# Kernel optimization log

Hardware: AMD Instinct MI355X
Metric: run time of the kernel (lower is better)

## Reference

```python
import jax, jax.numpy as jnp
import numpy as np

B, T, E, NH = 2, 2048, 512, 8
HD = E // NH
SCALE = float(HD) ** -0.5


def setup_inputs() -> dict:
    key = jax.random.key(0)
    ks = jax.random.split(key, 7)
    s = 0.02
    return {
        "x": jax.random.normal(ks[0], (B, T, E), dtype=jnp.float32),
        "w_qkv": jax.random.normal(ks[1], (E, 3 * E), dtype=jnp.float32) * s,
        "b_qkv": jax.random.normal(ks[2], (3 * E,), dtype=jnp.float32) * s,
        "w_od": jax.random.normal(ks[3], (E, 2 * NH), dtype=jnp.float32) * s,
        "b_od": jax.random.normal(ks[4], (2 * NH,), dtype=jnp.float32) * s,
        "w_out": jax.random.normal(ks[5], (E, E), dtype=jnp.float32) * s,
        "b_out": jax.random.normal(ks[6], (E,), dtype=jnp.float32) * s,
    }


def _heads(t):  # (B,T,E) -> (B*NH, T, HD)
    return t.reshape(B, T, NH, HD).transpose(0, 2, 1, 3).reshape(B * NH, T, HD)


def _point_mask(idx, j):  # idx: (B*NH,T) float indices -> one-hot (B*NH,T,T)
    return (j[None, None, :] == idx[:, :, None]).astype(jnp.float32)


def reference(x, w_qkv, b_qkv, w_od, b_od, w_out, b_out):
    qkv = x @ w_qkv + b_qkv
    Q, K, V = jnp.split(qkv, 3, axis=-1)  # each (B,T,E)

    od = Q @ w_od + b_od  # (B,T,2*NH)
    offset, duration = jnp.split(od, 2, axis=-1)
    offset = jnp.tanh(offset) * T
    duration = jax.nn.sigmoid(duration) * T

    query_index = jnp.arange(T, dtype=x.dtype)[None, :, None]  # (1,T,1)
    anchor = query_index + offset  # (B,T,NH)
    # 'b t nh -> (b nh) t'
    anchor = anchor.transpose(0, 2, 1).reshape(B * NH, T)
    duration = duration.transpose(0, 2, 1).reshape(B * NH, T)

    start = anchor - duration
    end = anchor + duration
    bound_l = jnp.floor(start)
    bound_r = jnp.ceil(end)
    anchor_l = jnp.floor(anchor)
    anchor_r = anchor_l + 1.0

    j = jnp.arange(T, dtype=x.dtype)
    neg_bound_weight = (bound_l - start)[:, :, None] * _point_mask(bound_l, j) \
                     + (end - bound_r)[:, :, None] * _point_mask(bound_r, j)
    anchor_dist_l = anchor - anchor_l
    anchor_weight = anchor_dist_l[:, :, None] * _point_mask(anchor_r, j) \
                  + (1.0 - anchor_dist_l)[:, :, None] * _point_mask(anchor_l, j)
    point_weight = 1.0 + neg_bound_weight + anchor_weight  # (B*NH,T,T)

    # segment mask: True OUTSIDE [bound_l, bound_r]
    attn_mask = (j[None, None, :] < bound_l[:, :, None]) | (j[None, None, :] > bound_r[:, :, None])

    Qh, Kh, Vh = _heads(Q), _heads(K), _heads(V)  # (B*NH, T, HD)
    scores = jnp.einsum('bic,brc->bir', Qh, Kh) * SCALE * point_weight
    scores = jnp.where(attn_mask, jnp.asarray(-1e8, scores.dtype), scores)
    attn = jax.nn.softmax(scores, axis=-1)
    out = jnp.einsum('bir,brc->bic', attn, Vh)  # (B*NH,T,HD)
    out = out.reshape(B, NH, T, HD).transpose(0, 2, 1, 3).reshape(B, T, E)
    return out @ w_out + b_out
```

## Files before the change

### kernel.cpp

```cpp
#include <hip/hip_runtime.h>
#include <math.h>

typedef float vf4 __attribute__((ext_vector_type(4)));
typedef float f32x4 __attribute__((ext_vector_type(4)));
typedef short bf16x8 __attribute__((ext_vector_type(8)));
typedef short short4v __attribute__((ext_vector_type(4)));
typedef int int2v __attribute__((ext_vector_type(2)));
typedef int int4v __attribute__((ext_vector_type(4)));

constexpr int B = 2, T = 2048, E = 512, NH = 8, HD = 64;
constexpr int BH = B * NH;
constexpr int NT = BH * T;
constexpr float SCALE = 0.125f;
constexpr float LOG2E = 1.44269504088896f;
constexpr float QSC = SCALE * LOG2E;

static __device__ __forceinline__ short f2bf(float f) {
  unsigned u = __float_as_uint(f);
  unsigned r = (u + 0x7fffu + ((u >> 16) & 1u)) >> 16;
  return (short)r;
}
static __device__ __forceinline__ unsigned pk2bf(float a, float b) {
  unsigned lo = (unsigned)(unsigned short)f2bf(a);
  unsigned hi = (unsigned)(unsigned short)f2bf(b);
  return lo | (hi << 16);
}
static __device__ __forceinline__ unsigned pkhu(float a, float b) {
  unsigned ua = __float_as_uint(a) + 0x8000u;
  unsigned ub = __float_as_uint(b) + 0x8000u;
  return __builtin_amdgcn_perm(ub, ua, 0x07060302u);
}
#if __has_builtin(__builtin_amdgcn_exp2f)
#define EXP2F(x) __builtin_amdgcn_exp2f(x)
#else
#define EXP2F(x) exp2f(x)
#endif
static __device__ __forceinline__ float bf2f(short s) {
  return __uint_as_float(((unsigned)(unsigned short)s) << 16);
}

__global__ __launch_bounds__(256) void prep_all(
    const float* __restrict__ x, const float* __restrict__ w_qkv,
    const float* __restrict__ b_qkv, const float* __restrict__ w_od,
    const float* __restrict__ b_od,
    short* __restrict__ xb, short* __restrict__ wTq, short* __restrict__ wTo,
    const float* __restrict__ w_out, float* __restrict__ Wc,
    float* __restrict__ bc)
{
  __shared__ float sh[8464];
  const int bid = blockIdx.x;
  const int tid = threadIdx.x;

  if (bid < 2048) {
    int idx = (bid * 256 + tid) * 4;
    vf4 v = *(const vf4*)&x[idx];
    short4v o;
    o[0] = f2bf(v[0]); o[1] = f2bf(v[1]); o[2] = f2bf(v[2]); o[3] = f2bf(v[3]);
    *(short4v*)&xb[idx] = o;
  } else if (bid < 3072) {
    const float* w; short* wT; int N, t;
    if (bid < 2816) { t = bid - 2048; w = w_qkv; wT = wTq; N = 1536; }
    else            { t = bid - 2816; w = w_out; wT = wTo; N = 512; }
    float (*tt)[33] = (float(*)[33])sh;
    const int k0 = (t & 15) * 32;
    const int n0 = (t >> 4) * 32;
    const int c = tid & 31, r = tid >> 5;
#pragma unroll
    for (int p = 0; p < 4; ++p)
      tt[r + p * 8][c] = w[(size_t)(k0 + r + p * 8) * N + n0 + c];
    __syncthreads();
#pragma unroll
    for (int p = 0; p < 4; ++p)
      wT[(size_t)(n0 + r + p * 8) * 512 + k0 + c] = f2bf(tt[c][r + p * 8]);
  } else {
    float* Lod = sh;
    float (*pb)[17] = (float(*)[17])(sh + 8192);
    const int bx = bid - 3072;
#pragma unroll
    for (int p = 0; p < 8; ++p) {
      int idx = (p * 256 + tid) * 4;
      *(vf4*)&Lod[idx] = *(const vf4*)&w_od[idx];
    }
    __syncthreads();
    if (bx < 32) {
      const int k = bx * 16 + (tid >> 4);
      const int c = tid & 15;
      float s = 0.0f;
      for (int m = 0; m < E; m += 4) {
        vf4 wq = *(const vf4*)&w_qkv[(size_t)k * 1536 + m];
        s += wq[0] * Lod[(m + 0) * 16 + c] + wq[1] * Lod[(m + 1) * 16 + c]
           + wq[2] * Lod[(m + 2) * 16 + c] + wq[3] * Lod[(m + 3) * 16 + c];
      }
      Wc[k * 16 + c] = s;
    } else {
      const int c = tid & 15, seg = tid >> 4;
      float s = 0.0f;
      for (int m = seg * 32; m < seg * 32 + 32; ++m)
        s += b_qkv[m] * Lod[m * 16 + c];
      pb[seg][c] = s;
      __syncthreads();
      if (tid < 16) {
        float acc = b_od[tid];
#pragma unroll
        for (int g = 0; g < 16; ++g) acc += pb[g][tid];
        bc[tid] = acc;
      }
    }
  }
}

__global__ __launch_bounds__(256) void qkv_gemm_bf16(
    const short* __restrict__ xb, const short* __restrict__ wT,
    const float* __restrict__ bias, short* __restrict__ qkvb,
    short* __restrict__ Vtg)
{
  __shared__ __align__(16) short As[128 * 40];
  __shared__ __align__(16) short Bt[128 * 40];

  const int tid = threadIdx.x;
  const int wave = tid >> 6, lane = tid & 63;
  const int quad = lane >> 4, l15 = lane & 15;
  const int wm = wave >> 1, wn = wave & 1;
  const int m0 = blockIdx.y * 128, n0 = blockIdx.x * 128;

  f32x4 acc[4][4];
#pragma unroll
  for (int mi = 0; mi < 4; ++mi)
#pragma unroll
    for (int ni = 0; ni < 4; ++ni) acc[mi][ni] = (f32x4){0, 0, 0, 0};

  const int sr = tid >> 1, sc = (tid & 1) * 16;

#pragma unroll 1
  for (int k0 = 0; k0 < E; k0 += 32) {
    __syncthreads();
    *(bf16x8*)&As[sr * 40 + sc] =
        *(const bf16x8*)&xb[(size_t)(m0 + sr) * 512 + k0 + sc];
    *(bf16x8*)&As[sr * 40 + sc + 8] =
        *(const bf16x8*)&xb[(size_t)(m0 + sr) * 512 + k0 + sc + 8];
    *(bf16x8*)&Bt[sr * 40 + sc] =
        *(const bf16x8*)&wT[(size_t)(n0 + sr) * 512 + k0 + sc];
    *(bf16x8*)&Bt[sr * 40 + sc + 8] =
        *(const bf16x8*)&wT[(size_t)(n0 + sr) * 512 + k0 + sc + 8];
    __syncthreads();

    bf16x8 aA[4], bB[4];
#pragma unroll
    for (int mi = 0; mi < 4; ++mi)
      aA[mi] = *(const bf16x8*)&As[(wm * 64 + mi * 16 + l15) * 40 + quad * 8];
#pragma unroll
    for (int ni = 0; ni < 4; ++ni)
      bB[ni] = *(const bf16x8*)&Bt[(wn * 64 + ni * 16 + l15) * 40 + quad * 8];
#pragma unroll
    for (int mi = 0; mi < 4; ++mi)
#pragma unroll
      for (int ni = 0; ni < 4; ++ni)
        acc[mi][ni] = __builtin_amdgcn_mfma_f32_16x16x32_bf16(
            aA[mi], bB[ni], acc[mi][ni], 0, 0, 0);
  }

#pragma unroll
  for (int mi = 0; mi < 4; ++mi)
#pragma unroll
    for (int ni = 0; ni < 4; ++ni) {
      const int col = n0 + wn * 64 + ni * 16 + l15;
      const int rowb = m0 + wm * 64 + mi * 16 + quad * 4;
      const float bs = bias[col];
      if (col < 1024) {
        const float qs = (col < 512) ? QSC : 1.0f;
#pragma unroll
        for (int r = 0; r < 4; ++r)
          qkvb[(size_t)(rowb + r) * 1536 + col] = f2bf((acc[mi][ni][r] + bs) * qs);
      } else {
        const int h = (col - 1024) >> 6, hd = col & 63;
        const int b = rowb >> 11, tt = rowb & 2047;
        int2v pk;
        pk[0] = (int)pk2bf(acc[mi][ni][0] + bs, acc[mi][ni][1] + bs);
        pk[1] = (int)pk2bf(acc[mi][ni][2] + bs, acc[mi][ni][3] + bs);
        *(int2v*)&Vtg[(size_t)(((b << 3) + h) * 64 + hd) * T + tt] = pk;
      }
    }
}

__global__ __launch_bounds__(256) void od_params(
    const float* __restrict__ x, const float* __restrict__ Wc,
    const float* __restrict__ bc, float* __restrict__ prm)
{
  __shared__ float od_s[16][16];
  const int tid = threadIdx.x;
  const int r = tid >> 4, c = tid & 15;
  const int row = blockIdx.x * 16 + r;

  float sum = bc[c];
  const float* qr = x + (size_t)row * E;
  for (int k = 0; k < E; k += 4) {
    vf4 q = *(const vf4*)&qr[k];
    sum += q[0] * Wc[(k + 0) * 16 + c]
         + q[1] * Wc[(k + 1) * 16 + c]
         + q[2] * Wc[(k + 2) * 16 + c]
         + q[3] * Wc[(k + 3) * 16 + c];
  }
  od_s[r][c] = sum;
  __syncthreads();

  if (tid < 128) {
    const int rr = tid >> 3, h = tid & 7;
    const int grow = blockIdx.x * 16 + rr;
    const int b = grow / T, i = grow % T;
    float o = od_s[rr][h];
    float d = od_s[rr][h + 8];
    float offset   = tanhf(o) * (float)T;
    float duration = (float)T / (1.0f + expf(-d));
    float anchor = (float)i + offset;
    float start = anchor - duration;
    float end   = anchor + duration;
    float bl = floorf(start);
    float br = ceilf(end);
    float al = floorf(anchor);
    float wbl = bl - start;
    float wbr = end - br;
    float af  = anchor - al;
    float rsc = 1.0f;
    if (br < 0.0f || bl > (float)(T - 1)) {
      bl = 0.0f; br = (float)(T - 1);
      wbl = 0.0f; wbr = 0.0f; al = -5.0f; af = 0.0f;
      rsc = 0.0f;
    }
    int idx = (b * NH + h) * T + i;
    prm[0 * NT + idx] = bl;
    prm[1 * NT + idx] = br;
    prm[2 * NT + idx] = wbl;
    prm[3 * NT + idx] = wbr;
    prm[4 * NT + idx] = al;
    prm[5 * NT + idx] = af;
    prm[6 * NT + idx] = rsc;
  }
}

__global__ __launch_bounds__(256, 4) void flash_attn_mfma4(
    const short* __restrict__ qkvb, const short* __restrict__ Vtg,
    const float* __restrict__ prm,
    short* __restrict__ Opart, float* __restrict__ lpart)
{
  __shared__ __align__(16) short Ks[64 * 72];
  __shared__ __align__(16) short Vt[64 * 72];
  __shared__ __align__(16) short Ps[4][16 * 72];
  __shared__ float u_s[8];

  const int tid = threadIdx.x;
  const int wave = tid >> 6, lane = tid & 63;
  const int quad = lane >> 4, l15 = lane & 15;
  const int qt = blockIdx.x, bh = blockIdx.y, ks = blockIdx.z;
  const int b = bh >> 3, h = bh & 7;
  const int i0 = qt * 64;
  const int i = i0 + wave * 16 + l15;

  const int pidx = bh * T + i;
  float blf = prm[0 * NT + pidx];
  float brf = prm[1 * NT + pidx];
  float wbl = prm[2 * NT + pidx];
  float wbr = prm[3 * NT + pidx];
  float alf = prm[4 * NT + pidx];
  float afr = prm[5 * NT + pidx];
  float rsc = prm[6 * NT + pidx];
  const int bli = (int)blf, widi = (int)brf - bli, ali = (int)alf;
  const unsigned widu = (unsigned)widi;
  const float a1 = 1.0f - afr;

  bf16x8 aQ0, aQ1;
  {
    size_t bq = (size_t)(b * T + i) * 1536 + h * 64;
    aQ0 = *(const bf16x8*)&qkvb[bq + quad * 8];
    aQ1 = *(const bf16x8*)&qkvb[bq + 32 + quad * 8];
    if (rsc == 0.0f) {
      bf16x8 z = {0, 0, 0, 0, 0, 0, 0, 0};
      aQ0 = z; aQ1 = z;
    }
  }

  float bmn = blf, bmx = brf;
#pragma unroll
  for (int d = 1; d < 64; d <<= 1) {
    bmn = fminf(bmn, __shfl_xor(bmn, d));
    bmx = fmaxf(bmx, __shfl_xor(bmx, d));
  }
  if (lane == 0) { u_s[wave * 2] = bmn; u_s[wave * 2 + 1] = bmx; }
  __syncthreads();
  bmn = fminf(fminf(u_s[0], u_s[2]), fminf(u_s[4], u_s[6]));
  bmx = fmaxf(fmaxf(u_s[1], u_s[3]), fmaxf(u_s[5], u_s[7]));
  const int ktlo = max(ks * 16, max(((int)bmn) >> 6, 0));
  const int kthi = min(ks * 16 + 15, min(((int)bmx) >> 6, T / 64 - 1));

  f32x4 o[4];
#pragma unroll
  for (int c = 0; c < 4; ++c) o[c] = (f32x4){0, 0, 0, 0};
  float lacc = 0.0f;

  const int rq = tid >> 3, cb = (tid & 7) * 8;

#pragma unroll 1
  for (int kt = ktlo; kt <= kthi; ++kt) {
    const int j0 = kt * 64;
    __syncthreads();
#pragma unroll
    for (int it = 0; it < 2; ++it) {
      int rr = it * 32 + rq;
      *(bf16x8*)&Ks[rr * 72 + cb] =
          *(const bf16x8*)&qkvb[(size_t)(b * T + j0 + rr) * 1536 + 512 + h * 64 + cb];
      *(bf16x8*)&Vt[rr * 72 + cb] =
          *(const bf16x8*)&Vtg[(size_t)(bh * 64 + rr) * T + j0 + cb];
    }
    __syncthreads();

    f32x4 s[4];
#pragma unroll
    for (int nc = 0; nc < 4; ++nc) {
      const short* kb = &Ks[(nc * 16 + l15) * 72 + quad * 8];
      f32x4 a = (f32x4){0, 0, 0, 0};
      a = __builtin_amdgcn_mfma_f32_16x16x32_bf16(*(const bf16x8*)&kb[0],  aQ0, a, 0, 0, 0);
      a = __builtin_amdgcn_mfma_f32_16x16x32_bf16(*(const bf16x8*)&kb[32], aQ1, a, 0, 0, 0);
      s[nc] = a;
    }

    const int clean = (bli < j0) & (bli + widi > j0 + 63) &
                      ((ali > j0 + 63) | (ali + 1 < j0));
    if (__all(clean)) {
#pragma unroll
      for (int nc = 0; nc < 4; ++nc) {
        float p0 = EXP2F(s[nc][0]);
        float p1 = EXP2F(s[nc][1]);
        float p2 = EXP2F(s[nc][2]);
        float p3 = EXP2F(s[nc][3]);
        lacc += (p0 + p1) + (p2 + p3);
        int2v pk;
        pk[0] = (int)pkhu(p0, p1);
        pk[1] = (int)pkhu(p2, p3);
        *(int2v*)&Ps[wave][l15 * 72 + nc * 16 + quad * 4] = pk;
      }
    } else {
      const int dq  = j0 + quad * 4 - bli;
      const int dq2 = j0 + quad * 4 - ali;
#pragma unroll
      for (int nc = 0; nc < 4; ++nc) {
        const int dn = dq + nc * 16, d2n = dq2 + nc * 16;
        float pr[4];
#pragma unroll
        for (int r = 0; r < 4; ++r) {
          int d = dn + r, d2 = d2n + r;
          float e  = (d == 0) ? wbl : ((d == widi) ? wbr : 0.0f);
          float aw = (d2 == 0) ? a1 : ((d2 == 1) ? afr : 0.0f);
          float w = 1.0f + e + aw;
          float v = s[nc][r] * w;
          v = ((unsigned)d <= widu) ? v : -115.0f;
          float p = EXP2F(v);
          lacc += p;
          pr[r] = p;
        }
        int2v pk;
        pk[0] = (int)pkhu(pr[0], pr[1]);
        pk[1] = (int)pkhu(pr[2], pr[3]);
        *(int2v*)&Ps[wave][l15 * 72 + nc * 16 + quad * 4] = pk;
      }
    }

    bf16x8 bP0 = *(const bf16x8*)&Ps[wave][l15 * 72 + quad * 8];
    bf16x8 bP1 = *(const bf16x8*)&Ps[wave][l15 * 72 + 32 + quad * 8];
#pragma unroll
    for (int nc2 = 0; nc2 < 4; ++nc2) {
      const short* vb = &Vt[(nc2 * 16 + l15) * 72 + quad * 8];
      o[nc2] = __builtin_amdgcn_mfma_f32_16x16x32_bf16(
          *(const bf16x8*)&vb[0],  bP0, o[nc2], 0, 0, 0);
      o[nc2] = __builtin_amdgcn_mfma_f32_16x16x32_bf16(
          *(const bf16x8*)&vb[32], bP1, o[nc2], 0, 0, 0);
    }
  }

  lacc += __shfl_xor(lacc, 16);
  lacc += __shfl_xor(lacc, 32);
  if (lane < 16)
    lpart[ks * NT + bh * T + i] = lacc;

  size_t ob = (size_t)ks * (B * T * E) + (size_t)(b * T + i) * E + h * 64;
#pragma unroll
  for (int nc2 = 0; nc2 < 4; ++nc2) {
    int2v pk;
    pk[0] = (int)pk2bf(o[nc2][0], o[nc2][1]);
    pk[1] = (int)pk2bf(o[nc2][2], o[nc2][3]);
    *(int2v*)&Opart[ob + nc2 * 16 + quad * 4] = pk;
  }
}

__global__ __launch_bounds__(256) void combine_attn(
    const short* __restrict__ Opart, const float* __restrict__ lpart,
    short* __restrict__ attnb)
{
  int base = (blockIdx.x * 256 + threadIdx.x) * 8;
  int row = base >> 9;
  int c = base & 511;
  int h = c >> 6;
  int b = row >> 11;
  int i = row & (T - 1);
  int lidx = ((b << 3) + h) * T + i;
  float inv = 1.0f / (lpart[lidx] + lpart[NT + lidx]);
  bf16x8 o0 = *(const bf16x8*)&Opart[base];
  bf16x8 o1 = *(const bf16x8*)&Opart[(size_t)(B * T * E) + base];
  int4v ov;
#pragma unroll
  for (int j = 0; j < 4; ++j) {
    float a = (bf2f(o0[2 * j]) + bf2f(o1[2 * j])) * inv;
    float bfv = (bf2f(o0[2 * j + 1]) + bf2f(o1[2 * j + 1])) * inv;
    ov[j] = (int)pk2bf(a, bfv);
  }
  *(int4v*)&attnb[base] = ov;
}

__global__ __launch_bounds__(256) void out_gemm_bf16(
    const short* __restrict__ Ab, const short* __restrict__ wT,
    const float* __restrict__ bias, float* __restrict__ Co)
{
  __shared__ __align__(16) short As[64 * 40];
  __shared__ __align__(16) short Bt[128 * 40];

  const int tid = threadIdx.x;
  const int wave = tid >> 6, lane = tid & 63;
  const int quad = lane >> 4, l15 = lane & 15;
  const int wm = wave >> 1, wn = wave & 1;
  const int m0 = blockIdx.y * 64, n0 = blockIdx.x * 128;

  f32x4 acc[2][4];
#pragma unroll
  for (int mi = 0; mi < 2; ++mi)
#pragma unroll
    for (int ni = 0; ni < 4; ++ni) acc[mi][ni] = (f32x4){0, 0, 0, 0};

  const int ar = tid >> 2, akc = (tid & 3) * 8;
  const int br_ = tid >> 1, bkc = (tid & 1) * 16;

#pragma unroll 1
  for (int k0 = 0; k0 < E; k0 += 32) {
    __syncthreads();
    *(bf16x8*)&As[ar * 40 + akc] =
        *(const bf16x8*)&Ab[(size_t)(m0 + ar) * 512 + k0 + akc];
    *(bf16x8*)&Bt[br_ * 40 + bkc] =
        *(const bf16x8*)&wT[(size_t)(n0 + br_) * 512 + k0 + bkc];
    *(bf16x8*)&Bt[br_ * 40 + bkc + 8] =
        *(const bf16x8*)&wT[(size_t)(n0 + br_) * 512 + k0 + bkc + 8];
    __syncthreads();

    bf16x8 aA[2], bB[4];
#pragma unroll
    for (int mi = 0; mi < 2; ++mi)
      aA[mi] = *(const bf16x8*)&As[(wm * 32 + mi * 16 + l15) * 40 + quad * 8];
#pragma unroll
    for (int ni = 0; ni < 4; ++ni)
      bB[ni] = *(const bf16x8*)&Bt[(wn * 64 + ni * 16 + l15) * 40 + quad * 8];
#pragma unroll
    for (int mi = 0; mi < 2; ++mi)
#pragma unroll
      for (int ni = 0; ni < 4; ++ni)
        acc[mi][ni] = __builtin_amdgcn_mfma_f32_16x16x32_bf16(
            aA[mi], bB[ni], acc[mi][ni], 0, 0, 0);
  }

#pragma unroll
  for (int mi = 0; mi < 2; ++mi)
#pragma unroll
    for (int ni = 0; ni < 4; ++ni)
#pragma unroll
      for (int r = 0; r < 4; ++r) {
        int row = m0 + wm * 32 + mi * 16 + quad * 4 + r;
        int col = n0 + wn * 64 + ni * 16 + l15;
        Co[(size_t)row * 512 + col] = acc[mi][ni][r] + bias[col];
      }
}

extern "C" void kernel_launch(void* const* d_in, const int* in_sizes, int n_in,
                              void* d_out, int out_size, void* d_ws, size_t ws_size,
                              hipStream_t stream)
{
  const float* x     = (const float*)d_in[0];
  const float* w_qkv = (const float*)d_in[1];
  const float* b_qkv = (const float*)d_in[2];
  const float* w_od  = (const float*)d_in[3];
  const float* b_od  = (const float*)d_in[4];
  const float* w_out = (const float*)d_in[5];
  const float* b_out = (const float*)d_in[6];
  float* out = (float*)d_out;

  char* w = (char*)d_ws;
  short* xb    = (short*)w;  w += (size_t)B * T * E * 2;
  short* wTq   = (short*)w;  w += (size_t)E * 3 * E * 2;
  short* wTo   = (short*)w;  w += (size_t)E * E * 2;
  short* qkvb  = (short*)w;  w += (size_t)B * T * 3 * E * 2;
  short* Vtg   = (short*)w;  w += (size_t)B * T * E * 2;
  float* Wc    = (float*)w;  w += (size_t)E * 16 * 4;
  float* bc    = (float*)w;  w += 256;
  float* prm   = (float*)w;  w += (size_t)7 * NT * 4;
  short* Opart = (short*)w;  w += (size_t)2 * B * T * E * 2;
  float* lpart = (float*)w;  w += (size_t)2 * NT * 4;
  short* attnb = (short*)w;  w += (size_t)B * T * E * 2;

  prep_all<<<dim3(3105), 256, 0, stream>>>(
      x, w_qkv, b_qkv, w_od, b_od, xb, wTq, wTo, w_out, Wc, bc);

  qkv_gemm_bf16<<<dim3(3 * E / 128, B * T / 128), 256, 0, stream>>>(
      xb, wTq, b_qkv, qkvb, Vtg);

  od_params<<<dim3(B * T / 16), 256, 0, stream>>>(x, Wc, bc, prm);

  flash_attn_mfma4<<<dim3(T / 64, BH, 2), 256, 0, stream>>>(
      qkvb, Vtg, prm, Opart, lpart);

  combine_attn<<<dim3(B * T * E / 2048), 256, 0, stream>>>(Opart, lpart, attnb);

  out_gemm_bf16<<<dim3(E / 128, B * T / 64), 256, 0, stream>>>(
      attnb, wTo, b_out, out);
}
```

Baseline: 183.2 us.

## Fuse QKV GEMM with OD params, double-buffer attention K/V, raise K-split to four

Merges the QKV GEMM and the offset/duration parameter kernel into one launch, shrinks the GEMM N-tile to 64 to get more blocks, and stages Wc in LDS for the param blocks. The attention kernel now double-buffers K/V tiles through registers and LDS so the next tile's loads overlap compute and only one barrier runs per iteration. The key split goes from 2 to 4 to raise parallelism, and the combine step sums four partials. The output GEMM tile also shrinks to 64x64 for more blocks. The cost is more partial-output traffic, extra LDS, and more but smaller GEMM blocks.

```diff
diff --git a/kernel.cpp b/kernel.cpp
--- a/kernel.cpp
+++ b/kernel.cpp
@@ -11,6 +11,7 @@
 constexpr int B = 2, T = 2048, E = 512, NH = 8, HD = 64;
 constexpr int BH = B * NH;
 constexpr int NT = BH * T;
+constexpr int KSPLIT = 4;
 constexpr float SCALE = 0.125f;
 constexpr float LOG2E = 1.44269504088896f;
 constexpr float QSC = SCALE * LOG2E;
@@ -109,141 +110,150 @@
   }
 }
 
-__global__ __launch_bounds__(256) void qkv_gemm_bf16(
+__global__ __launch_bounds__(256) void qkv_od(
     const short* __restrict__ xb, const short* __restrict__ wT,
     const float* __restrict__ bias, short* __restrict__ qkvb,
-    short* __restrict__ Vtg)
-{
-  __shared__ __align__(16) short As[128 * 40];
-  __shared__ __align__(16) short Bt[128 * 40];
-
-  const int tid = threadIdx.x;
-  const int wave = tid >> 6, lane = tid & 63;
-  const int quad = lane >> 4, l15 = lane & 15;
-  const int wm = wave >> 1, wn = wave & 1;
-  const int m0 = blockIdx.y * 128, n0 = blockIdx.x * 128;
-
-  f32x4 acc[4][4];
-#pragma unroll
-  for (int mi = 0; mi < 4; ++mi)
-#pragma unroll
-    for (int ni = 0; ni < 4; ++ni) acc[mi][ni] = (f32x4){0, 0, 0, 0};
-
-  const int sr = tid >> 1, sc = (tid & 1) * 16;
-
-#pragma unroll 1
-  for (int k0 = 0; k0 < E; k0 += 32) {
-    __syncthreads();
-    *(bf16x8*)&As[sr * 40 + sc] =
-        *(const bf16x8*)&xb[(size_t)(m0 + sr) * 512 + k0 + sc];
-    *(bf16x8*)&As[sr * 40 + sc + 8] =
-        *(const bf16x8*)&xb[(size_t)(m0 + sr) * 512 + k0 + sc + 8];
-    *(bf16x8*)&Bt[sr * 40 + sc] =
-        *(const bf16x8*)&wT[(size_t)(n0 + sr) * 512 + k0 + sc];
-    *(bf16x8*)&Bt[sr * 40 + sc + 8] =
-        *(const bf16x8*)&wT[(size_t)(n0 + sr) * 512 + k0 + sc + 8];
-    __syncthreads();
-
-    bf16x8 aA[4], bB[4];
-#pragma unroll
-    for (int mi = 0; mi < 4; ++mi)
-      aA[mi] = *(const bf16x8*)&As[(wm * 64 + mi * 16 + l15) * 40 + quad * 8];
-#pragma unroll
-    for (int ni = 0; ni < 4; ++ni)
-      bB[ni] = *(const bf16x8*)&Bt[(wn * 64 + ni * 16 + l15) * 40 + quad * 8];
-#pragma unroll
-    for (int mi = 0; mi < 4; ++mi)
-#pragma unroll
-      for (int ni = 0; ni < 4; ++ni)
-        acc[mi][ni] = __builtin_amdgcn_mfma_f32_16x16x32_bf16(
-            aA[mi], bB[ni], acc[mi][ni], 0, 0, 0);
-  }
-
-#pragma unroll
-  for (int mi = 0; mi < 4; ++mi)
-#pragma unroll
-    for (int ni = 0; ni < 4; ++ni) {
-      const int col = n0 + wn * 64 + ni * 16 + l15;
-      const int rowb = m0 + wm * 64 + mi * 16 + quad * 4;
-      const float bs = bias[col];
-      if (col < 1024) {
-        const float qs = (col < 512) ? QSC : 1.0f;
-#pragma unroll
-        for (int r = 0; r < 4; ++r)
-          qkvb[(size_t)(rowb + r) * 1536 + col] = f2bf((acc[mi][ni][r] + bs) * qs);
-      } else {
-        const int h = (col - 1024) >> 6, hd = col & 63;
-        const int b = rowb >> 11, tt = rowb & 2047;
-        int2v pk;
-        pk[0] = (int)pk2bf(acc[mi][ni][0] + bs, acc[mi][ni][1] + bs);
-        pk[1] = (int)pk2bf(acc[mi][ni][2] + bs, acc[mi][ni][3] + bs);
-        *(int2v*)&Vtg[(size_t)(((b << 3) + h) * 64 + hd) * T + tt] = pk;
-      }
-    }
-}
-
-__global__ __launch_bounds__(256) void od_params(
+    short* __restrict__ Vtg,
     const float* __restrict__ x, const float* __restrict__ Wc,
     const float* __restrict__ bc, float* __restrict__ prm)
 {
-  __shared__ float od_s[16][16];
+  __shared__ __align__(16) short smem_s[16896];
+  const int bid = blockIdx.x;
   const int tid = threadIdx.x;
-  const int r = tid >> 4, c = tid & 15;
-  const int row = blockIdx.x * 16 + r;
-
-  float sum = bc[c];
-  const float* qr = x + (size_t)row * E;
-  for (int k = 0; k < E; k += 4) {
-    vf4 q = *(const vf4*)&qr[k];
-    sum += q[0] * Wc[(k + 0) * 16 + c]
-         + q[1] * Wc[(k + 1) * 16 + c]
-         + q[2] * Wc[(k + 2) * 16 + c]
-         + q[3] * Wc[(k + 3) * 16 + c];
-  }
-  od_s[r][c] = sum;
-  __syncthreads();
-
-  if (tid < 128) {
-    const int rr = tid >> 3, h = tid & 7;
-    const int grow = blockIdx.x * 16 + rr;
-    const int b = grow / T, i = grow % T;
-    float o = od_s[rr][h];
-    float d = od_s[rr][h + 8];
-    float offset   = tanhf(o) * (float)T;
-    float duration = (float)T / (1.0f + expf(-d));
-    float anchor = (float)i + offset;
-    float start = anchor - duration;
-    float end   = anchor + duration;
-    float bl = floorf(start);
-    float br = ceilf(end);
-    float al = floorf(anchor);
-    float wbl = bl - start;
-    float wbr = end - br;
-    float af  = anchor - al;
-    float rsc = 1.0f;
-    if (br < 0.0f || bl > (float)(T - 1)) {
-      bl = 0.0f; br = (float)(T - 1);
-      wbl = 0.0f; wbr = 0.0f; al = -5.0f; af = 0.0f;
-      rsc = 0.0f;
-    }
-    int idx = (b * NH + h) * T + i;
-    prm[0 * NT + idx] = bl;
-    prm[1 * NT + idx] = br;
-    prm[2 * NT + idx] = wbl;
-    prm[3 * NT + idx] = wbr;
-    prm[4 * NT + idx] = al;
-    prm[5 * NT + idx] = af;
-    prm[6 * NT + idx] = rsc;
-  }
-}
-
-__global__ __launch_bounds__(256, 4) void flash_attn_mfma4(
+
+  if (bid < 768) {
+    short* As = smem_s;
+    short* Bt = smem_s + 128 * 40;
+    const int wave = tid >> 6, lane = tid & 63;
+    const int quad = lane >> 4, l15 = lane & 15;
+    const int wm = wave >> 1, wn = wave & 1;
+    const int bx = bid % 24, by = bid / 24;
+    const int m0 = by * 128, n0 = bx * 64;
+
+    f32x4 acc[4][2];
+#pragma unroll
+    for (int mi = 0; mi < 4; ++mi)
+#pragma unroll
+      for (int ni = 0; ni < 2; ++ni) acc[mi][ni] = (f32x4){0, 0, 0, 0};
+
+    const int sr = tid >> 1, sc = (tid & 1) * 16;
+    const int br2 = tid >> 2, bk2 = (tid & 3) * 8;
+
+#pragma unroll 1
+    for (int k0 = 0; k0 < E; k0 += 32) {
+      __syncthreads();
+      *(bf16x8*)&As[sr * 40 + sc] =
+          *(const bf16x8*)&xb[(size_t)(m0 + sr) * 512 + k0 + sc];
+      *(bf16x8*)&As[sr * 40 + sc + 8] =
+          *(const bf16x8*)&xb[(size_t)(m0 + sr) * 512 + k0 + sc + 8];
+      *(bf16x8*)&Bt[br2 * 40 + bk2] =
+          *(const bf16x8*)&wT[(size_t)(n0 + br2) * 512 + k0 + bk2];
+      __syncthreads();
+
+      bf16x8 aA[4], bB[2];
+#pragma unroll
+      for (int mi = 0; mi < 4; ++mi)
+        aA[mi] = *(const bf16x8*)&As[(wm * 64 + mi * 16 + l15) * 40 + quad * 8];
+#pragma unroll
+      for (int ni = 0; ni < 2; ++ni)
+        bB[ni] = *(const bf16x8*)&Bt[(wn * 32 + ni * 16 + l15) * 40 + quad * 8];
+#pragma unroll
+      for (int mi = 0; mi < 4; ++mi)
+#pragma unroll
+        for (int ni = 0; ni < 2; ++ni)
+          acc[mi][ni] = __builtin_amdgcn_mfma_f32_16x16x32_bf16(
+              aA[mi], bB[ni], acc[mi][ni], 0, 0, 0);
+    }
+
+#pragma unroll
+    for (int mi = 0; mi < 4; ++mi)
+#pragma unroll
+      for (int ni = 0; ni < 2; ++ni) {
+        const int col = n0 + wn * 32 + ni * 16 + l15;
+        const int rowb = m0 + wm * 64 + mi * 16 + quad * 4;
+        const float bs = bias[col];
+        if (col < 1024) {
+          const float qs = (col < 512) ? QSC : 1.0f;
+#pragma unroll
+          for (int r = 0; r < 4; ++r)
+            qkvb[(size_t)(rowb + r) * 1536 + col] =
+                f2bf((acc[mi][ni][r] + bs) * qs);
+        } else {
+          const int h = (col - 1024) >> 6, hd = col & 63;
+          const int b = rowb >> 11, tt = rowb & 2047;
+          int2v pk;
+          pk[0] = (int)pk2bf(acc[mi][ni][0] + bs, acc[mi][ni][1] + bs);
+          pk[1] = (int)pk2bf(acc[mi][ni][2] + bs, acc[mi][ni][3] + bs);
+          *(int2v*)&Vtg[(size_t)(((b << 3) + h) * 64 + hd) * T + tt] = pk;
+        }
+      }
+  } else {
+    float* Lod = (float*)smem_s;
+    float* ods = ((float*)smem_s) + 8192;
+    const int obx = bid - 768;
+#pragma unroll
+    for (int p = 0; p < 8; ++p) {
+      int idx = (p * 256 + tid) * 4;
+      *(vf4*)&Lod[idx] = *(const vf4*)&Wc[idx];
+    }
+    __syncthreads();
+
+    const int r = tid >> 4, c = tid & 15;
+    const int row = obx * 16 + r;
+    float sum = bc[c];
+    const float* qr = x + (size_t)row * E;
+    for (int k = 0; k < E; k += 4) {
+      vf4 q = *(const vf4*)&qr[k];
+      sum += q[0] * Lod[(k + 0) * 16 + c]
+           + q[1] * Lod[(k + 1) * 16 + c]
+           + q[2] * Lod[(k + 2) * 16 + c]
+           + q[3] * Lod[(k + 3) * 16 + c];
+    }
+    ods[r * 16 + c] = sum;
+    __syncthreads();
+
+    if (tid < 128) {
+      const int rr = tid >> 3, h = tid & 7;
+      const int grow = obx * 16 + rr;
+      const int b = grow / T, i = grow % T;
+      float o = ods[rr * 16 + h];
+      float d = ods[rr * 16 + h + 8];
+      float offset   = tanhf(o) * (float)T;
+      float duration = (float)T / (1.0f + expf(-d));
+      float anchor = (float)i + offset;
+      float start = anchor - duration;
+      float end   = anchor + duration;
+      float bl = floorf(start);
+      float br = ceilf(end);
+      float al = floorf(anchor);
+      float wbl = bl - start;
+      float wbr = end - br;
+      float af  = anchor - al;
+      float rsc = 1.0f;
+      if (br < 0.0f || bl > (float)(T - 1)) {
+        bl = 0.0f; br = (float)(T - 1);
+        wbl = 0.0f; wbr = 0.0f; al = -5.0f; af = 0.0f;
+        rsc = 0.0f;
+      }
+      int idx = (b * NH + h) * T + i;
+      prm[0 * NT + idx] = bl;
+      prm[1 * NT + idx] = br;
+      prm[2 * NT + idx] = wbl;
+      prm[3 * NT + idx] = wbr;
+      prm[4 * NT + idx] = al;
+      prm[5 * NT + idx] = af;
+      prm[6 * NT + idx] = rsc;
+    }
+  }
+}
+
+__global__ __launch_bounds__(256, 4) void flash_attn_mfma5(
     const short* __restrict__ qkvb, const short* __restrict__ Vtg,
     const float* __restrict__ prm,
     short* __restrict__ Opart, float* __restrict__ lpart)
 {
-  __shared__ __align__(16) short Ks[64 * 72];
-  __shared__ __align__(16) short Vt[64 * 72];
+  __shared__ __align__(16) short Ks[2][64 * 72];
+  __shared__ __align__(16) short Vt[2][64 * 72];
   __shared__ __align__(16) short Ps[4][16 * 72];
   __shared__ float u_s[8];
 
@@ -288,8 +298,8 @@
   __syncthreads();
   bmn = fminf(fminf(u_s[0], u_s[2]), fminf(u_s[4], u_s[6]));
   bmx = fmaxf(fmaxf(u_s[1], u_s[3]), fmaxf(u_s[5], u_s[7]));
-  const int ktlo = max(ks * 16, max(((int)bmn) >> 6, 0));
-  const int kthi = min(ks * 16 + 15, min(((int)bmx) >> 6, T / 64 - 1));
+  const int ktlo = max(ks * 8, max(((int)bmn) >> 6, 0));
+  const int kthi = min(ks * 8 + 7, min(((int)bmx) >> 6, T / 64 - 1));
 
   f32x4 o[4];
 #pragma unroll
@@ -297,25 +307,42 @@
   float lacc = 0.0f;
 
   const int rq = tid >> 3, cb = (tid & 7) * 8;
-
+  const short* kbase = qkvb + (size_t)b * T * 1536 + 512 + h * 64 + cb;
+  const short* vbase = Vtg + (size_t)bh * 64 * T + cb;
+
+  bf16x8 kr0, kr1, vr0, vr1;
+  if (ktlo <= kthi) {
+    const int j0 = ktlo * 64;
+    kr0 = *(const bf16x8*)&kbase[(size_t)(j0 + rq) * 1536];
+    kr1 = *(const bf16x8*)&kbase[(size_t)(j0 + 32 + rq) * 1536];
+    vr0 = *(const bf16x8*)&vbase[(size_t)rq * T + j0];
+    vr1 = *(const bf16x8*)&vbase[(size_t)(32 + rq) * T + j0];
+    *(bf16x8*)&Ks[0][rq * 72 + cb] = kr0;
+    *(bf16x8*)&Ks[0][(32 + rq) * 72 + cb] = kr1;
+    *(bf16x8*)&Vt[0][rq * 72 + cb] = vr0;
+    *(bf16x8*)&Vt[0][(32 + rq) * 72 + cb] = vr1;
+  }
+  __syncthreads();
+
+  int buf = 0;
 #pragma unroll 1
   for (int kt = ktlo; kt <= kthi; ++kt) {
     const int j0 = kt * 64;
-    __syncthreads();
-#pragma unroll
-    for (int it = 0; it < 2; ++it) {
-      int rr = it * 32 + rq;
-      *(bf16x8*)&Ks[rr * 72 + cb] =
-          *(const bf16x8*)&qkvb[(size_t)(b * T + j0 + rr) * 1536 + 512 + h * 64 + cb];
-      *(bf16x8*)&Vt[rr * 72 + cb] =
-          *(const bf16x8*)&Vtg[(size_t)(bh * 64 + rr) * T + j0 + cb];
-    }
-    __syncthreads();
+    if (kt < kthi) {
+      const int j1 = j0 + 64;
+      kr0 = *(const bf16x8*)&kbase[(size_t)(j1 + rq) * 1536];
+      kr1 = *(const bf16x8*)&kbase[(size_t)(j1 + 32 + rq) * 1536];
+      vr0 = *(const bf16x8*)&vbase[(size_t)rq * T + j1];
+      vr1 = *(const bf16x8*)&vbase[(size_t)(32 + rq) * T + j1];
+    }
+
+    const short* KsB = Ks[buf];
+    const short* VtB = Vt[buf];
 
     f32x4 s[4];
 #pragma unroll
     for (int nc = 0; nc < 4; ++nc) {
-      const short* kb = &Ks[(nc * 16 + l15) * 72 + quad * 8];
+      const short* kb = &KsB[(nc * 16 + l15) * 72 + quad * 8];
       f32x4 a = (f32x4){0, 0, 0, 0};
       a = __builtin_amdgcn_mfma_f32_16x16x32_bf16(*(const bf16x8*)&kb[0],  aQ0, a, 0, 0, 0);
       a = __builtin_amdgcn_mfma_f32_16x16x32_bf16(*(const bf16x8*)&kb[32], aQ1, a, 0, 0, 0);
@@ -367,11 +394,22 @@
     bf16x8 bP1 = *(const bf16x8*)&Ps[wave][l15 * 72 + 32 + quad * 8];
 #pragma unroll
     for (int nc2 = 0; nc2 < 4; ++nc2) {
-      const short* vb = &Vt[(nc2 * 16 + l15) * 72 + quad * 8];
+      const short* vb = &VtB[(nc2 * 16 + l15) * 72 + quad * 8];
       o[nc2] = __builtin_amdgcn_mfma_f32_16x16x32_bf16(
           *(const bf16x8*)&vb[0],  bP0, o[nc2], 0, 0, 0);
       o[nc2] = __builtin_amdgcn_mfma_f32_16x16x32_bf16(
           *(const bf16x8*)&vb[32], bP1, o[nc2], 0, 0, 0);
+    }
+
+    if (kt < kthi) {
+      short* Kn = Ks[buf ^ 1];
+      short* Vn = Vt[buf ^ 1];
+      *(bf16x8*)&Kn[rq * 72 + cb] = kr0;
+      *(bf16x8*)&Kn[(32 + rq) * 72 + cb] = kr1;
+      *(bf16x8*)&Vn[rq * 72 + cb] = vr0;
+      *(bf16x8*)&Vn[(32 + rq) * 72 + cb] = vr1;
+      __syncthreads();
+      buf ^= 1;
     }
   }
 
@@ -401,15 +439,21 @@
   int b = row >> 11;
   int i = row & (T - 1);
   int lidx = ((b << 3) + h) * T + i;
-  float inv = 1.0f / (lpart[lidx] + lpart[NT + lidx]);
+  float l = (lpart[lidx] + lpart[NT + lidx]) +
+            (lpart[2 * NT + lidx] + lpart[3 * NT + lidx]);
+  float inv = 1.0f / l;
   bf16x8 o0 = *(const bf16x8*)&Opart[base];
   bf16x8 o1 = *(const bf16x8*)&Opart[(size_t)(B * T * E) + base];
+  bf16x8 o2 = *(const bf16x8*)&Opart[(size_t)(2 * B * T * E) + base];
+  bf16x8 o3 = *(const bf16x8*)&Opart[(size_t)(3 * B * T * E) + base];
   int4v ov;
 #pragma unroll
   for (int j = 0; j < 4; ++j) {
-    float a = (bf2f(o0[2 * j]) + bf2f(o1[2 * j])) * inv;
-    float bfv = (bf2f(o0[2 * j + 1]) + bf2f(o1[2 * j + 1])) * inv;
-    ov[j] = (int)pk2bf(a, bfv);
+    float a = ((bf2f(o0[2 * j]) + bf2f(o1[2 * j])) +
+               (bf2f(o2[2 * j]) + bf2f(o3[2 * j]))) * inv;
+    float bb = ((bf2f(o0[2 * j + 1]) + bf2f(o1[2 * j + 1])) +
+                (bf2f(o2[2 * j + 1]) + bf2f(o3[2 * j + 1]))) * inv;
+    ov[j] = (int)pk2bf(a, bb);
   }
   *(int4v*)&attnb[base] = ov;
 }
@@ -419,45 +463,42 @@
     const float* __restrict__ bias, float* __restrict__ Co)
 {
   __shared__ __align__(16) short As[64 * 40];
-  __shared__ __align__(16) short Bt[128 * 40];
+  __shared__ __align__(16) short Bt[64 * 40];
 
   const int tid = threadIdx.x;
   const int wave = tid >> 6, lane = tid & 63;
   const int quad = lane >> 4, l15 = lane & 15;
   const int wm = wave >> 1, wn = wave & 1;
-  const int m0 = blockIdx.y * 64, n0 = blockIdx.x * 128;
-
-  f32x4 acc[2][4];
+  const int m0 = blockIdx.y * 64, n0 = blockIdx.x * 64;
+
+  f32x4 acc[2][2];
 #pragma unroll
   for (int mi = 0; mi < 2; ++mi)
 #pragma unroll
-    for (int ni = 0; ni < 4; ++ni) acc[mi][ni] = (f32x4){0, 0, 0, 0};
+    for (int ni = 0; ni < 2; ++ni) acc[mi][ni] = (f32x4){0, 0, 0, 0};
 
   const int ar = tid >> 2, akc = (tid & 3) * 8;
-  const int br_ = tid >> 1, bkc = (tid & 1) * 16;
 
 #pragma unroll 1
   for (int k0 = 0; k0 < E; k0 += 32) {
     __syncthreads();
     *(bf16x8*)&As[ar * 40 + akc] =
         *(const bf16x8*)&Ab[(size_t)(m0 + ar) * 512 + k0 + akc];
-    *(bf16x8*)&Bt[br_ * 40 + bkc] =
-        *(const bf16x8*)&wT[(size_t)(n0 + br_) * 512 + k0 + bkc];
-    *(bf16x8*)&Bt[br_ * 40 + bkc + 8] =
-        *(const bf16x8*)&wT[(size_t)(n0 + br_) * 512 + k0 + bkc + 8];
+    *(bf16x8*)&Bt[ar * 40 + akc] =
+        *(const bf16x8*)&wT[(size_t)(n0 + ar) * 512 + k0 + akc];
     __syncthreads();
 
-    bf16x8 aA[2], bB[4];
+    bf16x8 aA[2], bB[2];
 #pragma unroll
     for (int mi = 0; mi < 2; ++mi)
       aA[mi] = *(const bf16x8*)&As[(wm * 32 + mi * 16 + l15) * 40 + quad * 8];
 #pragma unroll
-    for (int ni = 0; ni < 4; ++ni)
-      bB[ni] = *(const bf16x8*)&Bt[(wn * 64 + ni * 16 + l15) * 40 + quad * 8];
+    for (int ni = 0; ni < 2; ++ni)
+      bB[ni] = *(const bf16x8*)&Bt[(wn * 32 + ni * 16 + l15) * 40 + quad * 8];
 #pragma unroll
     for (int mi = 0; mi < 2; ++mi)
 #pragma unroll
-      for (int ni = 0; ni < 4; ++ni)
+      for (int ni = 0; ni < 2; ++ni)
         acc[mi][ni] = __builtin_amdgcn_mfma_f32_16x16x32_bf16(
             aA[mi], bB[ni], acc[mi][ni], 0, 0, 0);
   }
@@ -465,11 +506,11 @@
 #pragma unroll
   for (int mi = 0; mi < 2; ++mi)
 #pragma unroll
-    for (int ni = 0; ni < 4; ++ni)
+    for (int ni = 0; ni < 2; ++ni)
 #pragma unroll
       for (int r = 0; r < 4; ++r) {
         int row = m0 + wm * 32 + mi * 16 + quad * 4 + r;
-        int col = n0 + wn * 64 + ni * 16 + l15;
+        int col = n0 + wn * 32 + ni * 16 + l15;
         Co[(size_t)row * 512 + col] = acc[mi][ni][r] + bias[col];
       }
 }
@@ -496,23 +537,21 @@
   float* Wc    = (float*)w;  w += (size_t)E * 16 * 4;
   float* bc    = (float*)w;  w += 256;
   float* prm   = (float*)w;  w += (size_t)7 * NT * 4;
-  short* Opart = (short*)w;  w += (size_t)2 * B * T * E * 2;
-  float* lpart = (float*)w;  w += (size_t)2 * NT * 4;
+  short* Opart = (short*)w;  w += (size_t)KSPLIT * B * T * E * 2;
+  float* lpart = (float*)w;  w += (size_t)KSPLIT * NT * 4;
   short* attnb = (short*)w;  w += (size_t)B * T * E * 2;
 
   prep_all<<<dim3(3105), 256, 0, stream>>>(
       x, w_qkv, b_qkv, w_od, b_od, xb, wTq, wTo, w_out, Wc, bc);
 
-  qkv_gemm_bf16<<<dim3(3 * E / 128, B * T / 128), 256, 0, stream>>>(
-      xb, wTq, b_qkv, qkvb, Vtg);
-
-  od_params<<<dim3(B * T / 16), 256, 0, stream>>>(x, Wc, bc, prm);
-
-  flash_attn_mfma4<<<dim3(T / 64, BH, 2), 256, 0, stream>>>(
+  qkv_od<<<dim3(1024), 256, 0, stream>>>(
+      xb, wTq, b_qkv, qkvb, Vtg, x, Wc, bc, prm);
+
+  flash_attn_mfma5<<<dim3(T / 64, BH, KSPLIT), 256, 0, stream>>>(
       qkvb, Vtg, prm, Opart, lpart);
 
   combine_attn<<<dim3(B * T * E / 2048), 256, 0, stream>>>(Opart, lpart, attnb);
 
-  out_gemm_bf16<<<dim3(E / 128, B * T / 64), 256, 0, stream>>>(
+  out_gemm_bf16<<<dim3(E / 64, B * T / 64), 256, 0, stream>>>(
       attnb, wTo, b_out, out);
 }
```

Result: faster. 163.6 us (-10.7%).
